# Kernel tuning notes

Hardware: AMD Instinct MI355X
Metric: run time of the kernel (lower is better)

Reference implementation:

```python
import jax, jax.numpy as jnp
import numpy as np

C1, C2, K, R = 32, 16, 3, 2
N, H, W, D = 2, 32, 32, 32


def _conv3d(x, w, b, pad):
    y = jax.lax.conv_general_dilated(
        x, w, window_strides=(1, 1, 1), padding=[(pad, pad)] * 3,
        dimension_numbers=('NCDHW', 'OIDHW', 'NCDHW'))
    return y + b[None, :, None, None, None]


def setup_inputs() -> dict:
    key = jax.random.key(0)
    ks = jax.random.split(key, 4)
    def winit(k, sh, fan):
        return jax.random.normal(k, sh, jnp.float32) * (1.0 / np.sqrt(fan))
    cm = C1 // 4
    ck = R ** 3 * K ** 3
    return {
        'x': jax.random.normal(ks[0], (N, C1, H, W, D), jnp.float32),
        'w_down': winit(ks[1], (cm, C1, 1, 1, 1), C1),
        'b_down': jnp.zeros((cm,), jnp.float32),
        'w_enc': winit(ks[2], (ck, cm, K, K, K), cm * K ** 3),
        'b_enc': jnp.zeros((ck,), jnp.float32),
        'w_out': winit(ks[3], (C2, C1, 1, 1, 1), C1),
        'b_out': jnp.zeros((C2,), jnp.float32),
    }


def reference(x, w_down, b_down, w_enc, b_enc, w_out, b_out):
    k3, r3 = K ** 3, R ** 3
    n, c, h, wd, d = x.shape
    # kernel prediction branch
    t = _conv3d(x, w_down, b_down, 0)                       # [N, C/4, H, W, D]
    enc = _conv3d(t, w_enc, b_enc, K // 2)                  # [N, r^3*k^3, H, W, D]
    # pixel_shuffle(k^3 outer, r^3 inner) + softmax over k^3 + unfold-back == this:
    kern = enc.reshape(n, k3, r3, h, wd, d)
    kern = jax.nn.softmax(kern, axis=1)
    kern = kern.transpose(0, 3, 4, 5, 1, 2)                 # [N, H, W, D, k^3, r^3]
    # im2col of x, same flattening order as torch triple unfold (kh outer, kd inner)
    p = K // 2
    xp = jnp.pad(x, ((0, 0), (0, 0), (p, p), (p, p), (p, p)))
    patches = jnp.stack(
        [xp[:, :, i:i + h, j:j + wd, l:l + d]
         for i in range(K) for j in range(K) for l in range(K)],
        axis=-1)                                            # [N, C, H, W, D, k^3]
    out = jnp.einsum('nchwdk,nhwdkr->nchwdr', patches, kern)  # [N, C, H, W, D, r^3]
    # pixel shuffle 3D (channel layout: C outer, r^3 inner)
    out = out.reshape(n, c, h, wd, d, R, R, R)
    out = out.transpose(0, 1, 2, 5, 3, 6, 4, 7).reshape(n, c, h * R, wd * R, d * R)
    return _conv3d(out, w_out, b_out, 0)                    # [N, C2, H*R, W*R, D*R]
```

## Files before the change

### kernel.cpp

```cpp
#include <hip/hip_runtime.h>


typedef short bf16x8 __attribute__((ext_vector_type(8)));
typedef float f32x4 __attribute__((ext_vector_type(4)));
typedef float v2f __attribute__((ext_vector_type(2)));

#define PSTR 232
#define PSTRD 116
#define MSP 41616
#define HSP 1224
#define WSP 36

__device__ inline unsigned short f2b(float f) {
  union { float f; unsigned int i; } x;
  x.f = f;
  unsigned int u = x.i;
  return (unsigned short)((u + 0x7FFFu + ((u >> 16) & 1u)) >> 16);
}
__device__ inline v2f b2f2(unsigned int u) {
  union { unsigned int i; float f; } lo, hi;
  lo.i = u << 16;
  hi.i = u & 0xFFFF0000u;
  return (v2f){lo.f, hi.f};
}

__global__ __launch_bounds__(256) void setup_kernel(
    const float* __restrict__ x, const float* __restrict__ w_down,
    const float* __restrict__ b_down, const float* __restrict__ w_enc,
    const float* __restrict__ b_enc, const float* __restrict__ w_out,
    unsigned short* __restrict__ t, uint2* __restrict__ xo64,
    unsigned short* __restrict__ Wb) {
  int blk = blockIdx.x;
  if (blk < 256) {
    int idx = blk * 256 + threadIdx.x;
    int n = idx >> 15, p = idx & 32767;
    int h = p >> 10, w = (p >> 5) & 31, d = p & 31;
    const float* xp = x + ((size_t)n << 20) + p;
    float at[8], ao[16];
#pragma unroll
    for (int m = 0; m < 8; ++m) at[m] = b_down[m];
#pragma unroll
    for (int o = 0; o < 16; ++o) ao[o] = 0.f;
#pragma unroll
    for (int c = 0; c < 32; ++c) {
      float xv = xp[(size_t)c << 15];
#pragma unroll
      for (int m = 0; m < 8; ++m) at[m] = fmaf(xv, w_down[m * 32 + c], at[m]);
#pragma unroll
      for (int o = 0; o < 16; ++o) ao[o] = fmaf(xv, w_out[o * 32 + c], ao[o]);
    }
    size_t spt = (size_t)(h + 1) * HSP + (size_t)(w + 1) * WSP + (d + 2);
#pragma unroll
    for (int m = 0; m < 8; ++m) t[(size_t)(n * 8 + m) * MSP + spt] = f2b(at[m]);
    size_t spx = (size_t)(h + 1) * HSP + (size_t)(w + 1) * WSP + (d + 1);
#pragma unroll
    for (int cq = 0; cq < 4; ++cq) {
      unsigned lo = (unsigned)f2b(ao[4 * cq]) | ((unsigned)f2b(ao[4 * cq + 1]) << 16);
      unsigned hi = (unsigned)f2b(ao[4 * cq + 2]) | ((unsigned)f2b(ao[4 * cq + 3]) << 16);
      xo64[(size_t)(n * 4 + cq) * MSP + spx] = make_uint2(lo, hi);
    }
  } else {
    int i = (blk - 256) * 256 + threadIdx.x;
    if (i < 224 * 224) {
      int o = i / 224;
      int k = i - o * 224;
      float v = 0.f;
      if (o < 216) {
        if (k < 216) v = w_enc[o * 216 + k];
        else if (k == 216) v = b_enc[o];
      }
      Wb[i] = f2b(v);
    }
  }
}

__global__ __launch_bounds__(256, 4) void carafe_kernel(
    const unsigned short* __restrict__ tg, const uint2* __restrict__ xog,
    const unsigned short* __restrict__ Wb, const float* __restrict__ b_out,
    float* __restrict__ y) {
  __shared__ __align__(16) unsigned short p_lds[64 * PSTR];
  __shared__ __align__(16) unsigned short t_lds[1728];
  __shared__ __align__(16) uint2 xo_lds[4 * 216];

  unsigned int* p32 = (unsigned int*)p_lds;
  unsigned int* t32 = (unsigned int*)t_lds;

  int pb = blockIdx.x;
  int G = ((pb >> 5) << 3) | (pb & 7);
  int q = (pb >> 3) & 3;
  int n = G >> 7;
  int h0 = ((G >> 4) & 7) << 2;
  int w0 = ((G >> 1) & 7) << 2;
  int d0 = ((G & 1) * 4 + q) << 2;
  int tid = threadIdx.x;

  for (int rr = tid; rr < 288; rr += 256) {
    int m = rr / 36;
    int rem = rr - m * 36;
    int z = rem / 6;
    int yy = rem - z * 6;
    size_t gsrc = (size_t)(n * 8 + m) * MSP + (size_t)(h0 + z) * HSP +
                  (size_t)(w0 + yy) * WSP + d0;
    uint2 l0 = *(const uint2*)(tg + gsrc);
    uint2 l1 = *(const uint2*)(tg + gsrc + 4);
    unsigned a = l0.x, b = l0.y, c = l1.x, e = l1.y;
    int dst = m * 108 + z * 18 + yy * 3;
    t32[dst] = (a >> 16) | (b << 16);
    t32[dst + 1] = (b >> 16) | (c << 16);
    t32[dst + 2] = (c >> 16) | (e << 16);
  }
  if (tid < 144) {
    int cq = tid / 36;
    int rem = tid - cq * 36;
    int z = rem / 6;
    int yy = rem - z * 6;
    size_t gsrc = (size_t)(n * 4 + cq) * MSP + (size_t)(h0 + z) * HSP +
                  (size_t)(w0 + yy) * WSP + d0;
    uint4 q0 = *(const uint4*)(xog + gsrc);
    uint4 q1 = *(const uint4*)(xog + gsrc + 2);
    uint4 q2 = *(const uint4*)(xog + gsrc + 4);
    int dst = cq * 216 + z * 36 + yy * 6;
    *(uint4*)&xo_lds[dst] = q0;
    *(uint4*)&xo_lds[dst + 2] = q1;
    *(uint4*)&xo_lds[dst + 4] = q2;
  }
  __syncthreads();

  int lane = tid & 63;
  int wv = __builtin_amdgcn_readfirstlane(tid >> 6);

  if (tid < 128) {
    int vp = tid >> 2, kq = tid & 3;
    int vA = vp * 2;
    int vz = vA >> 4, vy = (vA >> 2) & 3, vxh = (vA & 2) >> 1;
    unsigned int outA[27], outB[27];
#pragma unroll
    for (int j = 0; j < 27; ++j) { outA[j] = 0u; outB[j] = 0u; }
#pragma unroll
    for (int mi = 0; mi < 2; ++mi) {
      int m = kq * 2 + mi;
#pragma unroll
      for (int kh = 0; kh < 3; ++kh)
#pragma unroll
        for (int kw = 0; kw < 3; ++kw) {
          int rb = m * 108 + (vz + kh) * 18 + (vy + kw) * 3 + vxh;
          uint2 u = *(const uint2*)(t32 + rb);
          unsigned sA[3] = {u.x & 0xFFFFu, u.x >> 16, u.y & 0xFFFFu};
          unsigned sB[3] = {u.x >> 16, u.y & 0xFFFFu, u.y >> 16};
          int kl0 = mi * 27 + kh * 9 + kw * 3;
#pragma unroll
          for (int kd = 0; kd < 3; ++kd) {
            int kl = kl0 + kd;
            outA[kl >> 1] |= sA[kd] << (16 * (kl & 1));
            outB[kl >> 1] |= sB[kd] << (16 * (kl & 1));
          }
        }
    }
    unsigned int* pA = p32 + vA * PSTRD + kq * 27;
    unsigned int* pB = pA + PSTRD;
#pragma unroll
    for (int j = 0; j < 27; ++j) { pA[j] = outA[j]; pB[j] = outB[j]; }
  }
  if (tid < 64) {
    unsigned int* r = p32 + tid * PSTRD;
    r[108] = 0x3F80u;
    r[109] = 0u; r[110] = 0u; r[111] = 0u;
  }
  __syncthreads();

  int l15 = lane & 15;
  int quad = lane >> 4;
  int mh = wv >> 1;
  int nh = wv & 1;

  f32x4 acc[7][2];
#pragma unroll
  for (int i = 0; i < 7; ++i)
#pragma unroll
    for (int j = 0; j < 2; ++j) acc[i][j] = (f32x4){0.f, 0.f, 0.f, 0.f};
  {
    const unsigned short* Arow = Wb + (mh * 112 + l15) * 224 + quad * 8;
    const unsigned short* Bp = p_lds + (nh * 32 + l15) * PSTR + quad * 8;
#pragma unroll
    for (int kt = 0; kt < 7; ++kt) {
      bf16x8 bf0 = *(const bf16x8*)(Bp + kt * 32);
      bf16x8 bf1 = *(const bf16x8*)(Bp + 16 * PSTR + kt * 32);
#pragma unroll
      for (int i = 0; i < 7; ++i) {
        bf16x8 af = *(const bf16x8*)(Arow + i * 16 * 224 + kt * 32);
        acc[i][0] = __builtin_amdgcn_mfma_f32_16x16x32_bf16(af, bf0, acc[i][0], 0, 0, 0);
        acc[i][1] = __builtin_amdgcn_mfma_f32_16x16x32_bf16(af, bf1, acc[i][1], 0, 0, 0);
      }
    }
  }
  __syncthreads();

#pragma unroll
  for (int i = 0; i < 7; ++i) {
    int o = (mh * 7 + i) * 16 + quad * 4;
    if (o < 216) {
#pragma unroll
      for (int jn = 0; jn < 2; ++jn) {
        int vv = nh * 32 + jn * 16 + l15;
        unsigned lo = (unsigned)f2b(acc[i][jn][0]) | ((unsigned)f2b(acc[i][jn][1]) << 16);
        unsigned hi = (unsigned)f2b(acc[i][jn][2]) | ((unsigned)f2b(acc[i][jn][3]) << 16);
        *(uint2*)&p_lds[vv * PSTR + o] = make_uint2(lo, hi);
      }
    }
  }
  __syncthreads();

  {
    int vv = tid >> 2, rp = tid & 3;
    unsigned int* e = p32 + vv * PSTRD + rp;
    float v0[27], v1[27];
    float mx0 = -3.0e38f, mx1 = -3.0e38f;
#pragma unroll
    for (int k = 0; k < 27; ++k) {
      v2f f = b2f2(e[k * 4]);
      v0[k] = f.x; v1[k] = f.y;
      mx0 = fmaxf(mx0, f.x);
      mx1 = fmaxf(mx1, f.y);
    }
    float s0 = 0.f, s1 = 0.f;
#pragma unroll
    for (int k = 0; k < 27; ++k) {
      v0[k] = __expf(v0[k] - mx0);
      v1[k] = __expf(v1[k] - mx1);
      s0 += v0[k];
      s1 += v1[k];
    }
    float i0 = 1.0f / s0, i1 = 1.0f / s1;
#pragma unroll
    for (int k = 0; k < 27; ++k)
      e[k * 4] = (unsigned)f2b(v0[k] * i0) | ((unsigned)f2b(v1[k] * i1) << 16);
  }
  __syncthreads();

  int v4 = lane;
  int vz = v4 >> 4, vy = (v4 >> 2) & 3, vx = v4 & 3;
  int base = vz * 36 + vy * 6 + vx;
  int c2b = wv * 4;
  v2f accy[4][4];
#pragma unroll
  for (int i = 0; i < 4; ++i) {
    float bo = b_out[c2b + i];
#pragma unroll
    for (int j = 0; j < 4; ++j) accy[i][j] = (v2f){bo, bo};
  }
  const unsigned short* kb = p_lds + v4 * PSTR;
#pragma unroll
  for (int kh = 0; kh < 3; ++kh)
#pragma unroll
    for (int kw = 0; kw < 3; ++kw)
#pragma unroll
      for (int kd = 0; kd < 3; ++kd) {
        int k = kh * 9 + kw * 3 + kd;
        int off = base + kh * 36 + kw * 6 + kd;
        uint4 kw4 = *(const uint4*)(kb + k * 8);
        v2f kr[4];
        kr[0] = b2f2(kw4.x);
        kr[1] = b2f2(kw4.y);
        kr[2] = b2f2(kw4.z);
        kr[3] = b2f2(kw4.w);
        uint2 xq = xo_lds[wv * 216 + off];
        v2f x01 = b2f2(xq.x), x23 = b2f2(xq.y);
        float xv[4] = {x01.x, x01.y, x23.x, x23.y};
#pragma unroll
        for (int i = 0; i < 4; ++i) {
          v2f xs = (v2f){xv[i], xv[i]};
#pragma unroll
          for (int j = 0; j < 4; ++j)
            accy[i][j] = __builtin_elementwise_fma(xs, kr[j], accy[i][j]);
        }
      }

  int hh = (h0 + vz) << 1, ww = (w0 + vy) << 1, dd = (d0 + vx) << 1;
#pragma unroll
  for (int i = 0; i < 4; ++i) {
    size_t cb = ((size_t)(n * 16 + c2b + i)) << 18;
#pragma unroll
    for (int rh = 0; rh < 2; ++rh)
#pragma unroll
      for (int rw = 0; rw < 2; ++rw) {
        v2f a = accy[i][rh * 2 + rw];
        *(float2*)&y[cb + (size_t)((hh + rh) << 12) + ((ww + rw) << 6) + dd] =
            make_float2(a.x, a.y);
      }
  }
}

extern "C" void kernel_launch(void* const* d_in, const int* in_sizes, int n_in,
                              void* d_out, int out_size, void* d_ws, size_t ws_size,
                              hipStream_t stream) {
  const float* x      = (const float*)d_in[0];
  const float* w_down = (const float*)d_in[1];
  const float* b_down = (const float*)d_in[2];
  const float* w_enc  = (const float*)d_in[3];
  const float* b_enc  = (const float*)d_in[4];
  const float* w_out  = (const float*)d_in[5];
  const float* b_out  = (const float*)d_in[6];
  float* y = (float*)d_out;

  char* ws = (char*)d_ws;
  unsigned short* t    = (unsigned short*)(ws);
  uint2*          xo64 = (uint2*)(ws + 2663424);
  unsigned short* Wb   = (unsigned short*)(ws + 5326848);

  setup_kernel<<<dim3(452), dim3(256), 0, stream>>>(x, w_down, b_down, w_enc,
                                                    b_enc, w_out, t, xo64, Wb);
  carafe_kernel<<<dim3(1024), dim3(256), 0, stream>>>(t, xo64, Wb, b_out, y);
}
```

Measured before the change: 116.8 us.

## Double carafe tile to 128 voxels per block with 512 threads

New measurement: 113.1 us. 3.2% less time.

```diff
diff --git a/kernel.cpp b/kernel.cpp
--- a/kernel.cpp
+++ b/kernel.cpp
@@ -74,65 +74,56 @@
   }
 }
 
-__global__ __launch_bounds__(256, 4) void carafe_kernel(
+__global__ __launch_bounds__(512, 4) void carafe_kernel(
     const unsigned short* __restrict__ tg, const uint2* __restrict__ xog,
     const unsigned short* __restrict__ Wb, const float* __restrict__ b_out,
     float* __restrict__ y) {
-  __shared__ __align__(16) unsigned short p_lds[64 * PSTR];
-  __shared__ __align__(16) unsigned short t_lds[1728];
-  __shared__ __align__(16) uint2 xo_lds[4 * 216];
+  __shared__ __align__(16) unsigned short p_lds[128 * PSTR];
+  __shared__ __align__(16) unsigned int t32[1920];
+  __shared__ __align__(16) uint2 xo_lds[1728];
 
   unsigned int* p32 = (unsigned int*)p_lds;
-  unsigned int* t32 = (unsigned int*)t_lds;
 
   int pb = blockIdx.x;
-  int G = ((pb >> 5) << 3) | (pb & 7);
-  int q = (pb >> 3) & 3;
-  int n = G >> 7;
-  int h0 = ((G >> 4) & 7) << 2;
-  int w0 = ((G >> 1) & 7) << 2;
-  int d0 = ((G & 1) * 4 + q) << 2;
+  int n = pb >> 8;
+  int h0 = ((pb >> 4) & 15) << 1;
+  int w0 = ((pb >> 1) & 7) << 2;
+  int d0 = (pb & 1) << 4;
   int tid = threadIdx.x;
 
-  for (int rr = tid; rr < 288; rr += 256) {
-    int m = rr / 36;
-    int rem = rr - m * 36;
+  if (tid < 192) {
+    int m = tid / 24;
+    int rem = tid - m * 24;
     int z = rem / 6;
     int yy = rem - z * 6;
     size_t gsrc = (size_t)(n * 8 + m) * MSP + (size_t)(h0 + z) * HSP +
                   (size_t)(w0 + yy) * WSP + d0;
-    uint2 l0 = *(const uint2*)(tg + gsrc);
-    uint2 l1 = *(const uint2*)(tg + gsrc + 4);
-    unsigned a = l0.x, b = l0.y, c = l1.x, e = l1.y;
-    int dst = m * 108 + z * 18 + yy * 3;
-    t32[dst] = (a >> 16) | (b << 16);
-    t32[dst + 1] = (b >> 16) | (c << 16);
-    t32[dst + 2] = (c >> 16) | (e << 16);
-  }
-  if (tid < 144) {
-    int cq = tid / 36;
-    int rem = tid - cq * 36;
-    int z = rem / 6;
-    int yy = rem - z * 6;
-    size_t gsrc = (size_t)(n * 4 + cq) * MSP + (size_t)(h0 + z) * HSP +
-                  (size_t)(w0 + yy) * WSP + d0;
-    uint4 q0 = *(const uint4*)(xog + gsrc);
-    uint4 q1 = *(const uint4*)(xog + gsrc + 2);
-    uint4 q2 = *(const uint4*)(xog + gsrc + 4);
-    int dst = cq * 216 + z * 36 + yy * 6;
-    *(uint4*)&xo_lds[dst] = q0;
-    *(uint4*)&xo_lds[dst + 2] = q1;
-    *(uint4*)&xo_lds[dst + 4] = q2;
+    uint4 A = *(const uint4*)(tg + gsrc);
+    uint4 B = *(const uint4*)(tg + gsrc + 8);
+    uint2 C = *(const uint2*)(tg + gsrc + 16);
+    unsigned a[10] = {A.x, A.y, A.z, A.w, B.x, B.y, B.z, B.w, C.x, C.y};
+    int dst = tid * 10;
+#pragma unroll
+    for (int j = 0; j < 9; ++j) t32[dst + j] = (a[j] >> 16) | (a[j + 1] << 16);
+  } else if (tid < 288) {
+    int rr = tid - 192;
+    size_t gsrc = (size_t)(n * 4 + (rr / 24)) * MSP +
+                  (size_t)(h0 + ((rr / 6) & 3)) * HSP +
+                  (size_t)(w0 + (rr % 6)) * WSP + d0;
+    int dst = rr * 18;
+#pragma unroll
+    for (int j = 0; j < 9; ++j)
+      *(uint4*)&xo_lds[dst + 2 * j] = *(const uint4*)(xog + gsrc + 2 * j);
   }
   __syncthreads();
 
   int lane = tid & 63;
   int wv = __builtin_amdgcn_readfirstlane(tid >> 6);
 
-  if (tid < 128) {
+  if (tid < 256) {
     int vp = tid >> 2, kq = tid & 3;
     int vA = vp * 2;
-    int vz = vA >> 4, vy = (vA >> 2) & 3, vxh = (vA & 2) >> 1;
+    int vz = vA >> 6, vy = (vA >> 4) & 3, vxh = (vA & 15) >> 1;
     unsigned int outA[27], outB[27];
 #pragma unroll
     for (int j = 0; j < 27; ++j) { outA[j] = 0u; outB[j] = 0u; }
@@ -143,10 +134,10 @@
       for (int kh = 0; kh < 3; ++kh)
 #pragma unroll
         for (int kw = 0; kw < 3; ++kw) {
-          int rb = m * 108 + (vz + kh) * 18 + (vy + kw) * 3 + vxh;
-          uint2 u = *(const uint2*)(t32 + rb);
-          unsigned sA[3] = {u.x & 0xFFFFu, u.x >> 16, u.y & 0xFFFFu};
-          unsigned sB[3] = {u.x >> 16, u.y & 0xFFFFu, u.y >> 16};
+          int rb = ((m * 4 + vz + kh) * 6 + (vy + kw)) * 10 + vxh;
+          unsigned ux = t32[rb], uy = t32[rb + 1];
+          unsigned sA[3] = {ux & 0xFFFFu, ux >> 16, uy & 0xFFFFu};
+          unsigned sB[3] = {ux >> 16, uy & 0xFFFFu, uy >> 16};
           int kl0 = mi * 27 + kh * 9 + kw * 3;
 #pragma unroll
           for (int kd = 0; kd < 3; ++kd) {
@@ -161,7 +152,7 @@
 #pragma unroll
     for (int j = 0; j < 27; ++j) { pA[j] = outA[j]; pB[j] = outB[j]; }
   }
-  if (tid < 64) {
+  if (tid < 128) {
     unsigned int* r = p32 + tid * PSTRD;
     r[108] = 0x3F80u;
     r[109] = 0u; r[110] = 0u; r[111] = 0u;
@@ -170,8 +161,8 @@
 
   int l15 = lane & 15;
   int quad = lane >> 4;
-  int mh = wv >> 1;
-  int nh = wv & 1;
+  int mh = wv >> 2;
+  int nh = wv & 3;
 
   f32x4 acc[7][2];
 #pragma unroll
@@ -237,14 +228,13 @@
   }
   __syncthreads();
 
-  int v4 = lane;
-  int vz = v4 >> 4, vy = (v4 >> 2) & 3, vx = v4 & 3;
-  int base = vz * 36 + vy * 6 + vx;
-  int c2b = wv * 4;
+  int cq = wv >> 1;
+  int v4 = ((wv & 1) << 6) | lane;
+  int vz = v4 >> 6, vy = (v4 >> 4) & 3, vx = v4 & 15;
   v2f accy[4][4];
 #pragma unroll
   for (int i = 0; i < 4; ++i) {
-    float bo = b_out[c2b + i];
+    float bo = b_out[cq * 4 + i];
 #pragma unroll
     for (int j = 0; j < 4; ++j) accy[i][j] = (v2f){bo, bo};
   }
@@ -256,14 +246,14 @@
 #pragma unroll
       for (int kd = 0; kd < 3; ++kd) {
         int k = kh * 9 + kw * 3 + kd;
-        int off = base + kh * 36 + kw * 6 + kd;
+        int off = ((cq * 4 + vz + kh) * 6 + (vy + kw)) * 18 + (vx + kd);
         uint4 kw4 = *(const uint4*)(kb + k * 8);
         v2f kr[4];
         kr[0] = b2f2(kw4.x);
         kr[1] = b2f2(kw4.y);
         kr[2] = b2f2(kw4.z);
         kr[3] = b2f2(kw4.w);
-        uint2 xq = xo_lds[wv * 216 + off];
+        uint2 xq = xo_lds[off];
         v2f x01 = b2f2(xq.x), x23 = b2f2(xq.y);
         float xv[4] = {x01.x, x01.y, x23.x, x23.y};
 #pragma unroll
@@ -278,7 +268,7 @@
   int hh = (h0 + vz) << 1, ww = (w0 + vy) << 1, dd = (d0 + vx) << 1;
 #pragma unroll
   for (int i = 0; i < 4; ++i) {
-    size_t cb = ((size_t)(n * 16 + c2b + i)) << 18;
+    size_t cb = ((size_t)(n * 16 + cq * 4 + i)) << 18;
 #pragma unroll
     for (int rh = 0; rh < 2; ++rh)
 #pragma unroll
@@ -309,5 +299,5 @@
 
   setup_kernel<<<dim3(452), dim3(256), 0, stream>>>(x, w_down, b_down, w_enc,
                                                     b_enc, w_out, t, xo64, Wb);
-  carafe_kernel<<<dim3(1024), dim3(256), 0, stream>>>(t, xo64, Wb, b_out, y);
-}
+  carafe_kernel<<<dim3(512), dim3(512), 0, stream>>>(t, xo64, Wb, b_out, y);
+}
```
